# Performance work log

Hardware: AMD Instinct MI355X
Metric: run time of the kernel (lower is better)

Reference implementation:

```python
import jax, jax.numpy as jnp
import numpy as np

SEQ_LEN, BATCH, VOCAB = 64, 64, 10000
EMB, HID = 1024, 1024

def setup_inputs() -> dict:
    key = jax.random.key(0)
    ks = jax.random.split(key, 12)
    k = 1.0 / np.sqrt(HID)
    u = lambda kk, shape, a: jax.random.uniform(kk, shape, jnp.float32, -a, a)
    return {
        "inputs": jax.random.randint(ks[0], (SEQ_LEN, BATCH), 0, VOCAB),
        "hidden": jax.random.normal(ks[1], (2, BATCH, HID), jnp.float32),
        "emb": u(ks[2], (VOCAB, EMB), 0.1),
        "W0": u(ks[3], (HID, EMB), k),    # layer0 input weight (no bias)
        "Wh0": u(ks[4], (HID, HID), k),   # layer0 recurrent weight
        "b0": u(ks[5], (HID,), k),        # layer0 recurrent bias
        "W1": u(ks[6], (HID, HID), k),
        "Wh1": u(ks[7], (HID, HID), k),
        "b1": u(ks[8], (HID,), k),
        "Wd": u(ks[9], (VOCAB, HID), 0.1),
        "bd": jnp.zeros((VOCAB,), jnp.float32),
    }

def reference(inputs, hidden, emb, W0, Wh0, b0, W1, Wh1, b1, Wd, bd):
    # inputs: [S,B] int, hidden: [L=2,B,H]
    x = emb[inputs]  # [S,B,E]

    def step(h, xt):
        h0 = jnp.tanh(xt @ W0.T + h[0] @ Wh0.T + b0)     # [B,H]
        h1 = jnp.tanh(h0 @ W1.T + h[1] @ Wh1.T + b1)     # [B,H]
        logits_t = h1 @ Wd.T + bd                        # [B,V]
        return jnp.stack([h0, h1]), logits_t

    hidden_final, logits = jax.lax.scan(step, hidden, x)
    return logits, hidden_final
```

## Files before the change

kernel.cpp:

```cpp
#include <hip/hip_runtime.h>


#define S_LEN 64
#define BATCH 64
#define HID   1024
#define VOCAB 10000
#define VPAD  10240
#define SB    4096
#define SBV   40960000

typedef __attribute__((ext_vector_type(4))) float  f32x4;
typedef __attribute__((ext_vector_type(8))) __bf16 bf16x8;

__device__ inline unsigned short f2bf(float x) {
  union { float f; unsigned int u; } v; v.f = x;
  unsigned int r = v.u + 0x7fffu + ((v.u >> 16) & 1u);
  return (unsigned short)(r >> 16);
}
__device__ inline float bf2f(unsigned short s) {
  union { unsigned int u; float f; } v; v.u = ((unsigned int)s) << 16;
  return v.f;
}


__global__ __launch_bounds__(256) void prep_x(
    const int* __restrict__ inputs, const float* __restrict__ emb,
    unsigned short* __restrict__ Xbf) {
  int i = blockIdx.x * 256 + threadIdx.x;
  int row = i >> 8;
  int c4  = (i & 255) * 4;
  int tok = inputs[row];
  const float4 v = *reinterpret_cast<const float4*>(emb + (size_t)tok * HID + c4);
  unsigned short* o = Xbf + (size_t)row * HID + c4;
  o[0] = f2bf(v.x); o[1] = f2bf(v.y); o[2] = f2bf(v.z); o[3] = f2bf(v.w);
}

__global__ __launch_bounds__(256) void prep_w(
    const float* __restrict__ W0, const float* __restrict__ Wh0,
    const float* __restrict__ W1, const float* __restrict__ Wh1,
    unsigned short* __restrict__ W0bf, unsigned short* __restrict__ B0c,
    unsigned short* __restrict__ B1c) {
  int id = blockIdx.x * 256 + threadIdx.x;
  int n = id >> 10, k = id & 1023;
  W0bf[id] = f2bf(W0[id]);
  {
    float w = Wh0[id];
    unsigned short hi = f2bf(w);
    unsigned short lo = f2bf(w - bf2f(hi));
    size_t base = (size_t)n * 2048 + k;
    B0c[base] = hi; B0c[base + 1024] = lo;
  }
  {
    float w1 = W1[id], wh1 = Wh1[id];
    unsigned short h1i = f2bf(w1),  l1 = f2bf(w1 - bf2f(h1i));
    unsigned short hh  = f2bf(wh1), lh = f2bf(wh1 - bf2f(hh));
    size_t base = (size_t)n * 4096 + k;
    B1c[base]        = h1i; B1c[base + 1024] = hh;
    B1c[base + 2048] = l1;  B1c[base + 3072] = lh;
  }
}

__global__ __launch_bounds__(256) void prep_wd(
    const float* __restrict__ Wd, const float* __restrict__ bd,
    unsigned short* __restrict__ Wdbf, float* __restrict__ bdp) {
  int id = blockIdx.x * 256 + threadIdx.x;
  int row = id >> 10;
  Wdbf[id] = (row < VOCAB) ? f2bf(Wd[id]) : (unsigned short)0;
  if (id < VPAD) bdp[id] = (id < VOCAB) ? bd[id] : 0.0f;
}

__global__ __launch_bounds__(256) void prep_h(
    const float* __restrict__ hidden,
    unsigned short* __restrict__ A0b0,
    unsigned short* __restrict__ A1b0, unsigned short* __restrict__ A1b1) {
  int id = blockIdx.x * 256 + threadIdx.x;
  int b = id >> 10, n = id & 1023;
  float h0 = hidden[id];
  float h1 = hidden[BATCH * HID + id];
  unsigned short h0hi = f2bf(h0), h0lo = f2bf(h0 - bf2f(h0hi));
  unsigned short h1hi = f2bf(h1), h1lo = f2bf(h1 - bf2f(h1hi));
  size_t a0 = (size_t)b * 2048 + n;
  A0b0[a0] = h0hi; A0b0[a0 + 1024] = h0lo;
  size_t a1 = (size_t)b * 4096 + n;
  A1b0[a1 + 1024] = h1hi; A1b0[a1 + 3072] = h1lo;
  A1b1[a1 + 1024] = h1hi; A1b1[a1 + 3072] = h1lo;
}

__global__ __launch_bounds__(256) void gemm_bt_bias(
    const unsigned short* __restrict__ A, const unsigned short* __restrict__ B,
    const float* __restrict__ bias, float* __restrict__ C,
    int K, int N, int ldc) {
  unsigned bx = blockIdx.x, by = blockIdx.y;
  if ((gridDim.x & 7u) == 0u) {
    const unsigned lin = blockIdx.x + gridDim.x * blockIdx.y;
    const unsigned xpx = gridDim.x >> 3;
    const unsigned xcd = lin & 7u;
    const unsigned idx = lin >> 3;
    bx = xcd * xpx + idx % xpx;
    by = idx / xpx;
  }
  const int m0 = by * 128;
  const int n0 = bx * 128;
  __shared__ __align__(16) unsigned short As[128 * 64];
  __shared__ __align__(16) unsigned short Bs[128 * 64];
  const int tid = threadIdx.x;
  const int lane = tid & 63, w = tid >> 6;
  const int wm = w >> 1, wn = w & 1;
  f32x4 acc[4][4] = {};
  for (int k0 = 0; k0 < K; k0 += 64) {
#pragma unroll
    for (int i = 0; i < 4; ++i) {
      int off = i * 256 + tid;
      int row = off >> 3;
      int c8  = off & 7;
      __builtin_amdgcn_global_load_lds(
          (const __attribute__((address_space(1))) unsigned int*)(const void*)
              (A + (size_t)(m0 + row) * K + k0 + c8 * 8),
          (__attribute__((address_space(3))) unsigned int*)(void*)(As + (size_t)off * 8),
          16, 0, 0);
      __builtin_amdgcn_global_load_lds(
          (const __attribute__((address_space(1))) unsigned int*)(const void*)
              (B + (size_t)(n0 + row) * K + k0 + c8 * 8),
          (__attribute__((address_space(3))) unsigned int*)(void*)(Bs + (size_t)off * 8),
          16, 0, 0);
    }
    __syncthreads();
#pragma unroll
    for (int kk = 0; kk < 64; kk += 32) {
      bf16x8 af[4], bfr[4];
#pragma unroll
      for (int f = 0; f < 4; ++f) {
        int ar = wm * 64 + f * 16 + (lane & 15);
        int ac = kk + (lane >> 4) * 8;
        af[f]  = *reinterpret_cast<const bf16x8*>(&As[ar * 64 + ac]);
        int br = wn * 64 + f * 16 + (lane & 15);
        bfr[f] = *reinterpret_cast<const bf16x8*>(&Bs[br * 64 + ac]);
      }
#pragma unroll
      for (int i = 0; i < 4; ++i)
#pragma unroll
        for (int j = 0; j < 4; ++j)
          acc[i][j] = __builtin_amdgcn_mfma_f32_16x16x32_bf16(af[i], bfr[j], acc[i][j], 0, 0, 0);
    }
    __syncthreads();
  }
  const int rbase = (lane >> 4) * 4;
  const int cbase = lane & 15;
#pragma unroll
  for (int i = 0; i < 4; ++i) {
#pragma unroll
    for (int j = 0; j < 4; ++j) {
      int col = n0 + wn * 64 + j * 16 + cbase;
      if (col < N) {
        float bv = bias[col];
#pragma unroll
        for (int r = 0; r < 4; ++r) {
          int row = m0 + wm * 64 + i * 16 + rbase + r;
          C[(size_t)row * ldc + col] = acc[i][j][r] + bv;
        }
      }
    }
  }
}

__global__ __launch_bounds__(256) void phase_kernel(
    const unsigned short* __restrict__ A0,  unsigned short* __restrict__ A0n,
    const unsigned short* __restrict__ B0,  const float* __restrict__ U0t,
    const unsigned short* __restrict__ A1,  unsigned short* __restrict__ A1n,
    const unsigned short* __restrict__ B1,  const float* __restrict__ b1,
    unsigned short* __restrict__ H1t,
    float* __restrict__ h0f32, float* __restrict__ h1f32,
    int do0, int do1) {
  const int bid = blockIdx.x;
  const int layer = bid >> 8;
  if (layer == 0 && !do0) return;
  if (layer == 1 && !do1) return;
  const int lbid = bid & 255;
  const int xcd = lbid & 7;
  const int sub = lbid >> 3;
  const int m0 = (sub >> 3) << 4;
  const int n0 = xcd * 128 + ((sub & 7) << 4);
  const int tid = threadIdx.x, lane = tid & 63, w = tid >> 6;
  const int seg = layer ? 2048 : 1024;
  const int Ks  = seg >> 2;
  const int ld  = seg * 2;
  const unsigned short* Ap = layer ? A1 : A0;
  const unsigned short* Bp = layer ? B1 : B0;
  const int kbeg = w * Ks;
  const int arow = m0 + (lane & 15);
  const int brow = n0 + (lane & 15);
  const int koff = (lane >> 4) * 8;
  const unsigned short* aP = Ap + (size_t)arow * ld + kbeg + koff;
  const unsigned short* bP = Bp + (size_t)brow * ld + kbeg + koff;
  f32x4 acc = {0.f, 0.f, 0.f, 0.f};
#pragma unroll 4
  for (int kc = 0; kc < Ks; kc += 32) {
    bf16x8 ah = *reinterpret_cast<const bf16x8*>(aP + kc);
    bf16x8 al = *reinterpret_cast<const bf16x8*>(aP + seg + kc);
    bf16x8 bh = *reinterpret_cast<const bf16x8*>(bP + kc);
    bf16x8 bl = *reinterpret_cast<const bf16x8*>(bP + seg + kc);
    acc = __builtin_amdgcn_mfma_f32_16x16x32_bf16(ah, bh, acc, 0, 0, 0);
    acc = __builtin_amdgcn_mfma_f32_16x16x32_bf16(ah, bl, acc, 0, 0, 0);
    acc = __builtin_amdgcn_mfma_f32_16x16x32_bf16(al, bh, acc, 0, 0, 0);
  }
  __shared__ float red[4][256];
  const int rrow = (lane >> 4) * 4;
  const int ccol = lane & 15;
#pragma unroll
  for (int r = 0; r < 4; ++r) red[w][(rrow + r) * 16 + ccol] = acc[r];
  __syncthreads();
  {
    float v = red[0][tid] + red[1][tid] + red[2][tid] + red[3][tid];
    int b   = m0 + (tid >> 4);
    int col = n0 + (tid & 15);
    if (layer == 0) {
      float h = tanhf(v + U0t[(size_t)b * HID + col]);
      unsigned short hi = f2bf(h);
      unsigned short lo = f2bf(h - bf2f(hi));
      size_t a0 = (size_t)b * 2048 + col;
      A0n[a0] = hi; A0n[a0 + 1024] = lo;
      size_t a1 = (size_t)b * 4096 + col;
      A1n[a1] = hi; A1n[a1 + 2048] = lo;
      h0f32[(size_t)b * HID + col] = h;
    } else {
      float h = tanhf(v + b1[col]);
      unsigned short hi = f2bf(h);
      unsigned short lo = f2bf(h - bf2f(hi));
      size_t a1 = (size_t)b * 4096 + col;
      A1n[a1 + 1024] = hi; A1n[a1 + 3072] = lo;
      H1t[(size_t)b * HID + col] = hi;
      h1f32[(size_t)b * HID + col] = h;
    }
  }
}


extern "C" void kernel_launch(void* const* d_in, const int* in_sizes, int n_in,
                              void* d_out, int out_size, void* d_ws, size_t ws_size,
                              hipStream_t stream) {
  (void)in_sizes; (void)n_in; (void)out_size; (void)ws_size;
  const int*   inputs = (const int*)  d_in[0];
  const float* hidden = (const float*)d_in[1];
  const float* emb    = (const float*)d_in[2];
  const float* W0     = (const float*)d_in[3];
  const float* Wh0    = (const float*)d_in[4];
  const float* b0     = (const float*)d_in[5];
  const float* W1     = (const float*)d_in[6];
  const float* Wh1    = (const float*)d_in[7];
  const float* b1     = (const float*)d_in[8];
  const float* Wd     = (const float*)d_in[9];
  const float* bd     = (const float*)d_in[10];

  float*          U0  = (float*)d_out;
  unsigned short* Xbf = (unsigned short*)((char*)d_out + (size_t)16777216);

  char* ws = (char*)d_ws;
  size_t off = 0;
  auto alloc = [&](size_t bytes) { size_t p = off; off = (off + bytes + 255) & ~(size_t)255; return p; };
  unsigned short* W0bf = (unsigned short*)(ws + alloc((size_t)HID * HID * 2));
  unsigned short* Wdbf = (unsigned short*)(ws + alloc((size_t)VPAD * HID * 2));
  float*          bdp  = (float*)         (ws + alloc((size_t)VPAD * 4));
  unsigned short* B0c  = (unsigned short*)(ws + alloc((size_t)HID * 2048 * 2));
  unsigned short* B1c  = (unsigned short*)(ws + alloc((size_t)HID * 4096 * 2));
  unsigned short* H1bf = (unsigned short*)(ws + alloc((size_t)SB * HID * 2));
  unsigned short* A0b[2], *A1b[2];
  A0b[0] = (unsigned short*)(ws + alloc((size_t)BATCH * 2048 * 2));
  A0b[1] = (unsigned short*)(ws + alloc((size_t)BATCH * 2048 * 2));
  A1b[0] = (unsigned short*)(ws + alloc((size_t)BATCH * 4096 * 2));
  A1b[1] = (unsigned short*)(ws + alloc((size_t)BATCH * 4096 * 2));

  float* hid0 = (float*)d_out + (size_t)SBV;
  float* hid1 = hid0 + (size_t)BATCH * HID;

  prep_x <<<SB * HID / 4 / 256, 256, 0, stream>>>(inputs, emb, Xbf);
  prep_w <<<HID * HID / 256,    256, 0, stream>>>(W0, Wh0, W1, Wh1, W0bf, B0c, B1c);
  prep_wd<<<VPAD * HID / 256,   256, 0, stream>>>(Wd, bd, Wdbf, bdp);
  prep_h <<<BATCH * HID / 256,  256, 0, stream>>>(hidden, A0b[0], A1b[0], A1b[1]);

  gemm_bt_bias<<<dim3(HID / 128, SB / 128), 256, 0, stream>>>(
      Xbf, W0bf, b0, U0, HID, HID, HID);

  for (int t = 0; t <= S_LEN; ++t) {
    const float* U0t = U0 + (size_t)(t < S_LEN ? t : 0) * BATCH * HID;
    unsigned short* H1t = H1bf + (size_t)(t > 0 ? (t - 1) : 0) * BATCH * HID;
    phase_kernel<<<512, 256, 0, stream>>>(
        A0b[t & 1], A0b[(t + 1) & 1], B0c, U0t,
        A1b[t & 1], A1b[(t + 1) & 1], B1c, b1,
        H1t, hid0, hid1,
        (t < S_LEN) ? 1 : 0, (t > 0) ? 1 : 0);
  }

  gemm_bt_bias<<<dim3(VPAD / 128, SB / 128), 256, 0, stream>>>(
      H1bf, Wdbf, bdp, (float*)d_out, HID, VOCAB, VOCAB);
}
```

Baseline: 1.302 ms.

## Replace per-step recurrence launches with persistent cooperative kernel caching weights in LDS

The 65 per-timestep kernel launches are replaced by one cooperative persistent kernel of 192 blocks that loops over phases with grid.sync between them. Each block keeps a 16-row slice of its recurrent weight (hi/lo bf16 split) resident in LDS with an XOR swizzle, so weights are no longer re-read from global memory every step. Layer 1's input and recurrent GEMMs are split into separate block groups, with the W1·h0 partial sum staged through a ping-pong buffer, forming a three-stage pipeline. The cost is a grid-wide barrier per phase, 80KB of LDS per block, and only 192 blocks doing the work.

Result: slower. 2.561 ms (+96.7%).

```diff
diff --git a/kernel.cpp b/kernel.cpp
--- a/kernel.cpp
+++ b/kernel.cpp
@@ -1,4 +1,5 @@
 #include <hip/hip_runtime.h>
+#include <hip/hip_cooperative_groups.h>
 
 
 #define S_LEN 64
@@ -39,24 +40,25 @@
     const float* __restrict__ W0, const float* __restrict__ Wh0,
     const float* __restrict__ W1, const float* __restrict__ Wh1,
     unsigned short* __restrict__ W0bf, unsigned short* __restrict__ B0c,
-    unsigned short* __restrict__ B1c) {
+    unsigned short* __restrict__ B1a, unsigned short* __restrict__ B1b) {
   int id = blockIdx.x * 256 + threadIdx.x;
   int n = id >> 10, k = id & 1023;
   W0bf[id] = f2bf(W0[id]);
+  size_t base = (size_t)n * 2048 + k;
   {
     float w = Wh0[id];
     unsigned short hi = f2bf(w);
-    unsigned short lo = f2bf(w - bf2f(hi));
-    size_t base = (size_t)n * 2048 + k;
-    B0c[base] = hi; B0c[base + 1024] = lo;
+    B0c[base] = hi; B0c[base + 1024] = f2bf(w - bf2f(hi));
   }
   {
-    float w1 = W1[id], wh1 = Wh1[id];
-    unsigned short h1i = f2bf(w1),  l1 = f2bf(w1 - bf2f(h1i));
-    unsigned short hh  = f2bf(wh1), lh = f2bf(wh1 - bf2f(hh));
-    size_t base = (size_t)n * 4096 + k;
-    B1c[base]        = h1i; B1c[base + 1024] = hh;
-    B1c[base + 2048] = l1;  B1c[base + 3072] = lh;
+    float w = W1[id];
+    unsigned short hi = f2bf(w);
+    B1a[base] = hi; B1a[base + 1024] = f2bf(w - bf2f(hi));
+  }
+  {
+    float w = Wh1[id];
+    unsigned short hi = f2bf(w);
+    B1b[base] = hi; B1b[base + 1024] = f2bf(w - bf2f(hi));
   }
 }
 
@@ -71,19 +73,15 @@
 
 __global__ __launch_bounds__(256) void prep_h(
     const float* __restrict__ hidden,
-    unsigned short* __restrict__ A0b0,
-    unsigned short* __restrict__ A1b0, unsigned short* __restrict__ A1b1) {
+    unsigned short* __restrict__ A0x, unsigned short* __restrict__ A1x) {
   int id = blockIdx.x * 256 + threadIdx.x;
   int b = id >> 10, n = id & 1023;
   float h0 = hidden[id];
   float h1 = hidden[BATCH * HID + id];
-  unsigned short h0hi = f2bf(h0), h0lo = f2bf(h0 - bf2f(h0hi));
-  unsigned short h1hi = f2bf(h1), h1lo = f2bf(h1 - bf2f(h1hi));
-  size_t a0 = (size_t)b * 2048 + n;
-  A0b0[a0] = h0hi; A0b0[a0 + 1024] = h0lo;
-  size_t a1 = (size_t)b * 4096 + n;
-  A1b0[a1 + 1024] = h1hi; A1b0[a1 + 3072] = h1lo;
-  A1b1[a1 + 1024] = h1hi; A1b1[a1 + 3072] = h1lo;
+  unsigned short h0hi = f2bf(h0), h1hi = f2bf(h1);
+  size_t o = (size_t)b * 2048 + n;
+  A0x[o] = h0hi; A0x[o + 1024] = f2bf(h0 - bf2f(h0hi));
+  A1x[o] = h1hi; A1x[o + 1024] = f2bf(h1 - bf2f(h1hi));
 }
 
 __global__ __launch_bounds__(256) void gemm_bt_bias(
@@ -163,74 +161,138 @@
   }
 }
 
-__global__ __launch_bounds__(256) void phase_kernel(
-    const unsigned short* __restrict__ A0,  unsigned short* __restrict__ A0n,
-    const unsigned short* __restrict__ B0,  const float* __restrict__ U0t,
-    const unsigned short* __restrict__ A1,  unsigned short* __restrict__ A1n,
-    const unsigned short* __restrict__ B1,  const float* __restrict__ b1,
-    unsigned short* __restrict__ H1t,
-    float* __restrict__ h0f32, float* __restrict__ h1f32,
-    int do0, int do1) {
-  const int bid = blockIdx.x;
-  const int layer = bid >> 8;
-  if (layer == 0 && !do0) return;
-  if (layer == 1 && !do1) return;
-  const int lbid = bid & 255;
-  const int xcd = lbid & 7;
-  const int sub = lbid >> 3;
-  const int m0 = (sub >> 3) << 4;
-  const int n0 = xcd * 128 + ((sub & 7) << 4);
-  const int tid = threadIdx.x, lane = tid & 63, w = tid >> 6;
-  const int seg = layer ? 2048 : 1024;
-  const int Ks  = seg >> 2;
-  const int ld  = seg * 2;
-  const unsigned short* Ap = layer ? A1 : A0;
-  const unsigned short* Bp = layer ? B1 : B0;
-  const int kbeg = w * Ks;
-  const int arow = m0 + (lane & 15);
-  const int brow = n0 + (lane & 15);
-  const int koff = (lane >> 4) * 8;
-  const unsigned short* aP = Ap + (size_t)arow * ld + kbeg + koff;
-  const unsigned short* bP = Bp + (size_t)brow * ld + kbeg + koff;
-  f32x4 acc = {0.f, 0.f, 0.f, 0.f};
-#pragma unroll 4
-  for (int kc = 0; kc < Ks; kc += 32) {
-    bf16x8 ah = *reinterpret_cast<const bf16x8*>(aP + kc);
-    bf16x8 al = *reinterpret_cast<const bf16x8*>(aP + seg + kc);
-    bf16x8 bh = *reinterpret_cast<const bf16x8*>(bP + kc);
-    bf16x8 bl = *reinterpret_cast<const bf16x8*>(bP + seg + kc);
-    acc = __builtin_amdgcn_mfma_f32_16x16x32_bf16(ah, bh, acc, 0, 0, 0);
-    acc = __builtin_amdgcn_mfma_f32_16x16x32_bf16(ah, bl, acc, 0, 0, 0);
-    acc = __builtin_amdgcn_mfma_f32_16x16x32_bf16(al, bh, acc, 0, 0, 0);
-  }
-  __shared__ float red[4][256];
-  const int rrow = (lane >> 4) * 4;
-  const int ccol = lane & 15;
-#pragma unroll
-  for (int r = 0; r < 4; ++r) red[w][(rrow + r) * 16 + ccol] = acc[r];
+__global__ __launch_bounds__(256, 2) void rnn_persist(
+    const unsigned short* __restrict__ B0c,
+    const unsigned short* __restrict__ B1a,
+    const unsigned short* __restrict__ B1b,
+    const float* __restrict__ U0,
+    const float* __restrict__ b1,
+    unsigned short* __restrict__ A0x, unsigned short* __restrict__ A0y,
+    unsigned short* __restrict__ A1x, unsigned short* __restrict__ A1y,
+    float* __restrict__ P0, float* __restrict__ P1,
+    unsigned short* __restrict__ H1bf,
+    float* __restrict__ hid0, float* __restrict__ hid1) {
+  cooperative_groups::grid_group grid = cooperative_groups::this_grid();
+  extern __shared__ unsigned char smem[];
+  unsigned short* Wlds = (unsigned short*)smem;
+  float*          red  = (float*)(smem + 65536);
+
+  const int bid  = blockIdx.x;
+  const int type = bid >> 6;
+  const int nt   = bid & 63;
+  const int n0   = nt << 4;
+  const int tid  = threadIdx.x, lane = tid & 63, w = tid >> 6;
+
+  const unsigned short* Wsrc = (type == 0) ? B0c : (type == 1) ? B1a : B1b;
+  for (int c = tid; c < 4096; c += 256) {
+    int row = c >> 8;
+    int cc  = c & 255;
+    bf16x8 v = *reinterpret_cast<const bf16x8*>(Wsrc + (size_t)(n0 + row) * 2048 + cc * 8);
+    int sc = cc ^ (row & 7);
+    *reinterpret_cast<bf16x8*>(&Wlds[row * 2048 + sc * 8]) = v;
+  }
   __syncthreads();
-  {
-    float v = red[0][tid] + red[1][tid] + red[2][tid] + red[3][tid];
-    int b   = m0 + (tid >> 4);
-    int col = n0 + (tid & 15);
-    if (layer == 0) {
-      float h = tanhf(v + U0t[(size_t)b * HID + col]);
-      unsigned short hi = f2bf(h);
-      unsigned short lo = f2bf(h - bf2f(hi));
-      size_t a0 = (size_t)b * 2048 + col;
-      A0n[a0] = hi; A0n[a0 + 1024] = lo;
-      size_t a1 = (size_t)b * 4096 + col;
-      A1n[a1] = hi; A1n[a1 + 2048] = lo;
-      h0f32[(size_t)b * HID + col] = h;
-    } else {
-      float h = tanhf(v + b1[col]);
-      unsigned short hi = f2bf(h);
-      unsigned short lo = f2bf(h - bf2f(hi));
-      size_t a1 = (size_t)b * 4096 + col;
-      A1n[a1 + 1024] = hi; A1n[a1 + 3072] = lo;
-      H1t[(size_t)b * HID + col] = hi;
-      h1f32[(size_t)b * HID + col] = h;
+
+  const int kbeg = w << 8;
+  const int koff = (lane >> 4) << 3;
+  const int brow = lane & 15;
+  const int bswz = brow & 7;
+
+  const int em   = tid >> 2;
+  const int ecol = n0 + ((tid & 3) << 2);
+
+  for (int p = 0; p < 66; ++p) {
+    const int pm = p & 1;
+    const bool active = (type == 0) ? (p < 64)
+                      : (type == 1) ? (p >= 1 && p < 65)
+                      : (p >= 2);
+    if (active) {
+      const unsigned short* Aprev =
+          (type == 2) ? (pm ? A1y : A1x) : (pm ? A0y : A0x);
+
+      float4 pre = {0.f, 0.f, 0.f, 0.f};
+      float4 pre2 = {0.f, 0.f, 0.f, 0.f};
+      if (type == 0) {
+        pre = *reinterpret_cast<const float4*>(U0 + (size_t)p * (BATCH * HID) + em * HID + ecol);
+      } else if (type == 2) {
+        const float* Pp = pm ? P1 : P0;
+        pre  = *reinterpret_cast<const float4*>(Pp + em * HID + ecol);
+        pre2 = *reinterpret_cast<const float4*>(b1 + ecol);
+      }
+
+      f32x4 acc[4] = {};
+#pragma unroll 2
+      for (int kc = 0; kc < 256; kc += 32) {
+        int colh = kbeg + koff + kc;
+        int ch = (colh >> 3) ^ bswz;
+        int cl = ((colh + 1024) >> 3) ^ bswz;
+        bf16x8 bh = *reinterpret_cast<const bf16x8*>(&Wlds[brow * 2048 + ch * 8]);
+        bf16x8 bl = *reinterpret_cast<const bf16x8*>(&Wlds[brow * 2048 + cl * 8]);
+#pragma unroll
+        for (int i = 0; i < 4; ++i) {
+          const unsigned short* ap = Aprev + (size_t)(i * 16 + brow) * 2048 + colh;
+          bf16x8 ah = *reinterpret_cast<const bf16x8*>(ap);
+          bf16x8 al = *reinterpret_cast<const bf16x8*>(ap + 1024);
+          acc[i] = __builtin_amdgcn_mfma_f32_16x16x32_bf16(ah, bh, acc[i], 0, 0, 0);
+          acc[i] = __builtin_amdgcn_mfma_f32_16x16x32_bf16(ah, bl, acc[i], 0, 0, 0);
+          acc[i] = __builtin_amdgcn_mfma_f32_16x16x32_bf16(al, bh, acc[i], 0, 0, 0);
+        }
+      }
+
+      const int rrow = (lane >> 4) << 2;
+#pragma unroll
+      for (int i = 0; i < 4; ++i)
+#pragma unroll
+        for (int r = 0; r < 4; ++r)
+          red[w * 1024 + (i * 16 + rrow + r) * 16 + brow] = acc[i][r];
+      __syncthreads();
+
+      {
+        const int o = tid * 4;
+        float v0 = red[o]        + red[1024 + o]     + red[2048 + o]     + red[3072 + o];
+        float v1 = red[o + 1]    + red[1024 + o + 1] + red[2048 + o + 1] + red[3072 + o + 1];
+        float v2 = red[o + 2]    + red[1024 + o + 2] + red[2048 + o + 2] + red[3072 + o + 2];
+        float v3 = red[o + 3]    + red[1024 + o + 3] + red[2048 + o + 3] + red[3072 + o + 3];
+        if (type == 0) {
+          float h0v = tanhf(v0 + pre.x), h1v = tanhf(v1 + pre.y);
+          float h2v = tanhf(v2 + pre.z), h3v = tanhf(v3 + pre.w);
+          unsigned short* An = pm ? A0x : A0y;
+          ushort4 hv, lv;
+          hv.x = f2bf(h0v); lv.x = f2bf(h0v - bf2f(hv.x));
+          hv.y = f2bf(h1v); lv.y = f2bf(h1v - bf2f(hv.y));
+          hv.z = f2bf(h2v); lv.z = f2bf(h2v - bf2f(hv.z));
+          hv.w = f2bf(h3v); lv.w = f2bf(h3v - bf2f(hv.w));
+          *reinterpret_cast<ushort4*>(&An[(size_t)em * 2048 + ecol])        = hv;
+          *reinterpret_cast<ushort4*>(&An[(size_t)em * 2048 + 1024 + ecol]) = lv;
+          if (p == S_LEN - 1) {
+            float4 f; f.x = h0v; f.y = h1v; f.z = h2v; f.w = h3v;
+            *reinterpret_cast<float4*>(&hid0[(size_t)em * HID + ecol]) = f;
+          }
+        } else if (type == 1) {
+          float* Pn = pm ? P0 : P1;
+          float4 f; f.x = v0; f.y = v1; f.z = v2; f.w = v3;
+          *reinterpret_cast<float4*>(&Pn[(size_t)em * HID + ecol]) = f;
+        } else {
+          float h0v = tanhf(v0 + pre.x + pre2.x), h1v = tanhf(v1 + pre.y + pre2.y);
+          float h2v = tanhf(v2 + pre.z + pre2.z), h3v = tanhf(v3 + pre.w + pre2.w);
+          unsigned short* An = pm ? A1x : A1y;
+          ushort4 hv, lv;
+          hv.x = f2bf(h0v); lv.x = f2bf(h0v - bf2f(hv.x));
+          hv.y = f2bf(h1v); lv.y = f2bf(h1v - bf2f(hv.y));
+          hv.z = f2bf(h2v); lv.z = f2bf(h2v - bf2f(hv.z));
+          hv.w = f2bf(h3v); lv.w = f2bf(h3v - bf2f(hv.w));
+          *reinterpret_cast<ushort4*>(&An[(size_t)em * 2048 + ecol])        = hv;
+          *reinterpret_cast<ushort4*>(&An[(size_t)em * 2048 + 1024 + ecol]) = lv;
+          unsigned short* H1t = H1bf + (size_t)(p - 2) * (BATCH * HID);
+          *reinterpret_cast<ushort4*>(&H1t[(size_t)em * HID + ecol]) = hv;
+          if (p == 65) {
+            float4 f; f.x = h0v; f.y = h1v; f.z = h2v; f.w = h3v;
+            *reinterpret_cast<float4*>(&hid1[(size_t)em * HID + ecol]) = f;
+          }
+        }
+      }
     }
+    grid.sync();
   }
 }
 
@@ -261,33 +323,36 @@
   unsigned short* Wdbf = (unsigned short*)(ws + alloc((size_t)VPAD * HID * 2));
   float*          bdp  = (float*)         (ws + alloc((size_t)VPAD * 4));
   unsigned short* B0c  = (unsigned short*)(ws + alloc((size_t)HID * 2048 * 2));
-  unsigned short* B1c  = (unsigned short*)(ws + alloc((size_t)HID * 4096 * 2));
+  unsigned short* B1a  = (unsigned short*)(ws + alloc((size_t)HID * 2048 * 2));
+  unsigned short* B1b  = (unsigned short*)(ws + alloc((size_t)HID * 2048 * 2));
   unsigned short* H1bf = (unsigned short*)(ws + alloc((size_t)SB * HID * 2));
-  unsigned short* A0b[2], *A1b[2];
-  A0b[0] = (unsigned short*)(ws + alloc((size_t)BATCH * 2048 * 2));
-  A0b[1] = (unsigned short*)(ws + alloc((size_t)BATCH * 2048 * 2));
-  A1b[0] = (unsigned short*)(ws + alloc((size_t)BATCH * 4096 * 2));
-  A1b[1] = (unsigned short*)(ws + alloc((size_t)BATCH * 4096 * 2));
+  unsigned short* A0x  = (unsigned short*)(ws + alloc((size_t)BATCH * 2048 * 2));
+  unsigned short* A0y  = (unsigned short*)(ws + alloc((size_t)BATCH * 2048 * 2));
+  unsigned short* A1x  = (unsigned short*)(ws + alloc((size_t)BATCH * 2048 * 2));
+  unsigned short* A1y  = (unsigned short*)(ws + alloc((size_t)BATCH * 2048 * 2));
+  float*          P0   = (float*)         (ws + alloc((size_t)BATCH * HID * 4));
+  float*          P1   = (float*)         (ws + alloc((size_t)BATCH * HID * 4));
 
   float* hid0 = (float*)d_out + (size_t)SBV;
   float* hid1 = hid0 + (size_t)BATCH * HID;
 
   prep_x <<<SB * HID / 4 / 256, 256, 0, stream>>>(inputs, emb, Xbf);
-  prep_w <<<HID * HID / 256,    256, 0, stream>>>(W0, Wh0, W1, Wh1, W0bf, B0c, B1c);
+  prep_w <<<HID * HID / 256,    256, 0, stream>>>(W0, Wh0, W1, Wh1, W0bf, B0c, B1a, B1b);
   prep_wd<<<VPAD * HID / 256,   256, 0, stream>>>(Wd, bd, Wdbf, bdp);
-  prep_h <<<BATCH * HID / 256,  256, 0, stream>>>(hidden, A0b[0], A1b[0], A1b[1]);
+  prep_h <<<BATCH * HID / 256,  256, 0, stream>>>(hidden, A0x, A1x);
 
   gemm_bt_bias<<<dim3(HID / 128, SB / 128), 256, 0, stream>>>(
       Xbf, W0bf, b0, U0, HID, HID, HID);
 
-  for (int t = 0; t <= S_LEN; ++t) {
-    const float* U0t = U0 + (size_t)(t < S_LEN ? t : 0) * BATCH * HID;
-    unsigned short* H1t = H1bf + (size_t)(t > 0 ? (t - 1) : 0) * BATCH * HID;
-    phase_kernel<<<512, 256, 0, stream>>>(
-        A0b[t & 1], A0b[(t + 1) & 1], B0c, U0t,
-        A1b[t & 1], A1b[(t + 1) & 1], B1c, b1,
-        H1t, hid0, hid1,
-        (t < S_LEN) ? 1 : 0, (t > 0) ? 1 : 0);
+  {
+    const unsigned short* cB0c = B0c; const unsigned short* cB1a = B1a;
+    const unsigned short* cB1b = B1b; const float* cU0 = U0; const float* cb1 = b1;
+    void* args[] = {
+        (void*)&cB0c, (void*)&cB1a, (void*)&cB1b, (void*)&cU0, (void*)&cb1,
+        (void*)&A0x, (void*)&A0y, (void*)&A1x, (void*)&A1y,
+        (void*)&P0, (void*)&P1, (void*)&H1bf, (void*)&hid0, (void*)&hid1};
+    hipLaunchCooperativeKernel(reinterpret_cast<const void*>(&rnn_persist),
+                               dim3(192), dim3(256), args, 81920, stream);
   }
 
   gemm_bt_bias<<<dim3(VPAD / 128, SB / 128), 256, 0, stream>>>(
```
